# Kernel optimization log

Measured on AMD Instinct MI355X. Metric: run time of the kernel, lower is better.

The kernel has to match this reference:

```python
import jax, jax.numpy as jnp
import numpy as np
from jax.scipy.special import erfinv

EMBED = 384
HEADS = 6
HEAD_DIM = EMBED // HEADS  # 64
N_FREQS = HEAD_DIM // 2    # 32
SEQ = 1025                 # 1 CLS + 32*32 patches
POS_DIM = 2
MIN_FREQ, MAX_FREQ = 0.1, 1000.0


def _phi(m: int) -> float:
    x = 2.0
    for _ in range(10):
        x = (1.0 + x) ** (1.0 / (m + 1.0))
    return x


def _uniform_directions(n: int, d: int) -> jnp.ndarray:
    # golden-ratio quasi-random directions, normalized (matches uniform_directions_jax)
    g = _phi(d)
    alpha = (1.0 / g) ** jnp.arange(1, d + 1, dtype=jnp.float32)
    i = jnp.arange(1, n + 1, dtype=jnp.float32)[:, None]
    z = jnp.fmod(i * alpha, 1.0)
    dirs = erfinv(2.0 * z - 1.0)
    return dirs / jnp.linalg.norm(dirs, axis=1, keepdims=True)


def _rope_freqs() -> jnp.ndarray:  # [h, F, P]
    omega = MIN_FREQ * (MAX_FREQ / MIN_FREQ) ** jnp.linspace(0.0, 1.0, N_FREQS)
    dirs = _uniform_directions(HEADS * N_FREQS, POS_DIM).reshape(HEADS, N_FREQS, POS_DIM)
    return dirs * omega.reshape(1, N_FREQS, 1)


def _coords_2d() -> jnp.ndarray:  # [S, 2], CLS at origin, patches in [-1,1]^2
    n = int(np.sqrt(SEQ - 1))  # 32
    yy, xx = jnp.meshgrid(jnp.arange(n), jnp.arange(n), indexing='ij')
    xf = xx.flatten().astype(jnp.float32) / (n - 1) * 2 - 1
    yf = yy.flatten().astype(jnp.float32) / (n - 1) * 2 - 1
    patch = jnp.stack([xf, yf], axis=1)
    return jnp.concatenate([jnp.zeros((1, 2), jnp.float32), patch], axis=0)


def _apply_rope(t_bshd, freqs_hFP, coords_SP):
    # theta: [S, h, F]
    theta = jnp.einsum('hfp,sp->shf', freqs_hFP, coords_SP)
    cos, sin = jnp.cos(theta), jnp.sin(theta)  # broadcast over batch
    x1, y1 = jnp.split(t_bshd, 2, axis=-1)     # [b,s,h,F] each
    return jnp.concatenate([x1 * cos - y1 * sin, x1 * sin + y1 * cos], axis=-1)


def setup_inputs() -> dict:
    key = jax.random.key(0)
    ks = jax.random.split(key, 6)
    scale = 1.0 / np.sqrt(EMBED)
    return {
        'x':  jax.random.normal(ks[0], (16, SEQ, EMBED), jnp.float32),
        'Wq': jax.random.normal(ks[1], (EMBED, EMBED), jnp.float32) * scale,
        'Wk': jax.random.normal(ks[2], (EMBED, EMBED), jnp.float32) * scale,
        'Wv': jax.random.normal(ks[3], (EMBED, EMBED), jnp.float32) * scale,
        'Wo': jax.random.normal(ks[4], (EMBED, EMBED), jnp.float32) * scale,
        'bo': jnp.zeros((EMBED,), jnp.float32),
    }


def reference(x, Wq, Wk, Wv, Wo, bo):
    b, s, e = x.shape
    freqs = _rope_freqs()   # constant buffers
    coords = _coords_2d()
    q = (x @ Wq).reshape(b, s, HEADS, HEAD_DIM)
    k = (x @ Wk).reshape(b, s, HEADS, HEAD_DIM)
    v = (x @ Wv).reshape(b, s, HEADS, HEAD_DIM)
    q = _apply_rope(q, freqs, coords)
    k = _apply_rope(k, freqs, coords)
    scores = jnp.einsum('blhd,bmhd->bhlm', q, k) / np.sqrt(HEAD_DIM)
    attn = jax.nn.softmax(scores, axis=-1)
    out = jnp.einsum('bhlm,bmhd->blhd', attn, v).reshape(b, s, e)
    return out @ Wo + bo
```

## Files before the change

### kernel.cpp

```cpp
#include <hip/hip_runtime.h>
#include <hip/hip_bf16.h>
#include <math.h>

#define EMBED 384
#define HEADS 6
#define HD    64
#define NF    32
#define SEQ   1025
#define SEQP  1088
#define BATCH 16
#define MTOT  (BATCH*SEQ)
#define NCHUNK 17
#define LSTRIDE 72
#define GSTR 40

typedef __bf16 bf16x8 __attribute__((ext_vector_type(8)));
typedef __bf16 bf16x4 __attribute__((ext_vector_type(4)));
typedef float  f32x4  __attribute__((ext_vector_type(4)));

#define MFMA_BF16(A,B,C) __builtin_amdgcn_mfma_f32_16x16x32_bf16((A),(B),(C),0,0,0)

__device__ __forceinline__ __bf16 f2bf(float f){
    __hip_bfloat16 h = __float2bfloat16(f);
    return *reinterpret_cast<__bf16*>(&h);
}

__global__ __launch_bounds__(256) void x_to_bf16_kernel(
    const float* __restrict__ x, __hip_bfloat16* __restrict__ xb)
{
    const int n4 = MTOT*EMBED/4;
    int i = blockIdx.x*256 + threadIdx.x;
    if (i < n4){
        float4 v = *reinterpret_cast<const float4*>(x + (size_t)i*4);
        bf16x4 b; b[0]=f2bf(v.x); b[1]=f2bf(v.y); b[2]=f2bf(v.z); b[3]=f2bf(v.w);
        *reinterpret_cast<bf16x4*>(reinterpret_cast<__bf16*>(xb) + (size_t)i*4) = b;
    }
}

__global__ __launch_bounds__(256) void transpose_w_kernel(
    const float* __restrict__ Wq, const float* __restrict__ Wk,
    const float* __restrict__ Wv, const float* __restrict__ Wo,
    __hip_bfloat16* __restrict__ Wt)
{
    __shared__ float tile[64][65];
    const int mat = blockIdx.z;
    const float* W = (mat==0)?Wq:(mat==1)?Wk:(mat==2)?Wv:Wo;
    const int k0 = blockIdx.x*64, n0 = blockIdx.y*64;
    const int c = threadIdx.x & 63, rq = threadIdx.x >> 6;
    #pragma unroll
    for (int i = 0; i < 16; ++i){
        int row = rq*16 + i;
        tile[row][c] = W[(size_t)(k0+row)*EMBED + n0 + c];
    }
    __syncthreads();
    #pragma unroll
    for (int i = 0; i < 16; ++i){
        int nr = rq*16 + i;
        Wt[((size_t)mat*EMBED + n0 + nr)*EMBED + k0 + c] = __float2bfloat16(tile[c][nr]);
    }
}

__device__ __forceinline__ float erfinv_f(float x){
    float w = -log1pf(-x*x);
    float p;
    if (w < 5.0f){
        w -= 2.5f;
        p = 2.81022636e-08f;
        p = fmaf(p, w, 3.43273939e-07f);
        p = fmaf(p, w, -3.5233877e-06f);
        p = fmaf(p, w, -4.39150654e-06f);
        p = fmaf(p, w, 0.00021858087f);
        p = fmaf(p, w, -0.00125372503f);
        p = fmaf(p, w, -0.00417768164f);
        p = fmaf(p, w, 0.246640727f);
        p = fmaf(p, w, 1.50140941f);
    } else {
        w = sqrtf(w) - 3.0f;
        p = -0.000200214257f;
        p = fmaf(p, w, 0.000100950558f);
        p = fmaf(p, w, 0.00134934322f);
        p = fmaf(p, w, -0.00367342844f);
        p = fmaf(p, w, 0.00573950773f);
        p = fmaf(p, w, -0.0076224613f);
        p = fmaf(p, w, 0.00943887047f);
        p = fmaf(p, w, 1.00167406f);
        p = fmaf(p, w, 2.83297682f);
    }
    return p * x;
}

__global__ void rope_tables_kernel(float* __restrict__ cos_t, float* __restrict__ sin_t){
    int idx = blockIdx.x * blockDim.x + threadIdx.x;
    if (idx >= SEQ*HEADS*NF) return;
    int f  = idx & (NF-1);
    int hf = idx / NF;
    int h  = hf % HEADS;
    int s  = hf / HEADS;

    double xd = 2.0;
    #pragma unroll
    for (int it = 0; it < 10; ++it) xd = cbrt(1.0 + xd);
    float a1 = (float)(1.0 / xd);
    float a2 = a1 * a1;

    float fi = (float)(h*NF + f + 1);
    float z1 = fmodf(fi * a1, 1.0f);
    float z2 = fmodf(fi * a2, 1.0f);
    float d1 = erfinv_f(2.0f*z1 - 1.0f);
    float d2 = erfinv_f(2.0f*z2 - 1.0f);
    float inv = 1.0f / sqrtf(d1*d1 + d2*d2);
    d1 *= inv; d2 *= inv;

    float omega = 0.1f * powf(10000.0f, (float)f / 31.0f);
    float fx = d1 * omega, fy = d2 * omega;

    float cx = 0.0f, cy = 0.0f;
    if (s > 0){
        int pi = s - 1;
        cx = (float)(pi & 31) / 31.0f * 2.0f - 1.0f;
        cy = (float)(pi >> 5) / 31.0f * 2.0f - 1.0f;
    }
    float theta = fx*cx + fy*cy;
    float sv, cv;
    sincosf(theta, &sv, &cv);
    cos_t[idx] = cv;
    sin_t[idx] = sv;
}

__global__ __launch_bounds__(256, 3) void qkv_rope_kernel(
    const __hip_bfloat16* __restrict__ xb_,
    const __hip_bfloat16* __restrict__ Wt,
    const float* __restrict__ cos_t,
    const float* __restrict__ sin_t,
    __hip_bfloat16* __restrict__ qbuf,
    __hip_bfloat16* __restrict__ kbuf,
    __hip_bfloat16* __restrict__ vbuf)
{
    __shared__ __align__(16) __bf16 xs[128*GSTR];
    __shared__ __align__(16) __bf16 bt[128*GSTR];
    const int tid = threadIdx.x;
    const int m0 = blockIdx.x * 128;
    const int j  = blockIdx.y;
    const __bf16* xb = reinterpret_cast<const __bf16*>(xb_);
    const __bf16* wt = reinterpret_cast<const __bf16*>(Wt);

    int soff[2], arow[2], brow[2];
    #pragma unroll
    for (int i = 0; i < 2; ++i){
        int g = tid + i*256;
        int row = g >> 2, kc = g & 3;
        soff[i] = row*GSTR + kc*8;
        int am = m0 + row; if (am > MTOT-1) am = MTOT-1;
        arow[i] = am;
        brow[i] = j*128 + row;
    }

    bf16x8 ar[2], br[2];
    #pragma unroll
    for (int i = 0; i < 2; ++i){
        int g = tid + i*256, kc = g & 3;
        ar[i] = *reinterpret_cast<const bf16x8*>(xb + (size_t)arow[i]*EMBED + kc*8);
        br[i] = *reinterpret_cast<const bf16x8*>(wt + (size_t)brow[i]*EMBED + kc*8);
    }

    const int w = tid >> 6;
    const int lane = tid & 63;
    const int quad = lane >> 4, low = lane & 15;
    const int mh = w >> 1, nh = w & 1;
    const int mw0 = m0 + mh*64;

    f32x4 acc[4][4] = {};
    for (int kb = 0; kb < 12; ++kb){
        __syncthreads();
        #pragma unroll
        for (int i = 0; i < 2; ++i){
            *reinterpret_cast<bf16x8*>(&xs[soff[i]]) = ar[i];
            *reinterpret_cast<bf16x8*>(&bt[soff[i]]) = br[i];
        }
        __syncthreads();
        if (kb < 11){
            const int k1 = (kb+1)*32;
            #pragma unroll
            for (int i = 0; i < 2; ++i){
                int g = tid + i*256, kc = g & 3;
                ar[i] = *reinterpret_cast<const bf16x8*>(xb + (size_t)arow[i]*EMBED + k1 + kc*8);
                br[i] = *reinterpret_cast<const bf16x8*>(wt + (size_t)brow[i]*EMBED + k1 + kc*8);
            }
        }
        bf16x8 af[4], bfr[4];
        #pragma unroll
        for (int mt = 0; mt < 4; ++mt)
            af[mt] = *reinterpret_cast<const bf16x8*>(&xs[(mh*64 + mt*16 + low)*GSTR + quad*8]);
        #pragma unroll
        for (int t = 0; t < 4; ++t)
            bfr[t] = *reinterpret_cast<const bf16x8*>(&bt[(nh*64 + t*16 + low)*GSTR + quad*8]);
        #pragma unroll
        for (int t = 0; t < 4; ++t)
            #pragma unroll
            for (int mt = 0; mt < 4; ++mt)
                acc[mt][t] = MFMA_BF16(af[mt], bfr[t], acc[mt][t]);
    }

    const int n64 = j*2 + nh;
    const int mat = n64 / 6;
    const int h   = n64 % 6;

    if (mat == 2){
        #pragma unroll
        for (int mt = 0; mt < 4; ++mt)
            #pragma unroll
            for (int t = 0; t < 4; ++t)
                #pragma unroll
                for (int r = 0; r < 4; ++r){
                    int m = mw0 + mt*16 + quad*4 + r;
                    if (m < MTOT){
                        int b = m / SEQ, s = m % SEQ;
                        vbuf[((size_t)(b*HEADS + h)*SEQ + s)*HD + t*16 + low] = __float2bfloat16(acc[mt][t][r]);
                    }
                }
    } else {
        __hip_bfloat16* ob = (mat == 0) ? qbuf : kbuf;
        const float qs_ = (mat == 0) ? 0.125f : 1.0f;
        #pragma unroll
        for (int mt = 0; mt < 4; ++mt)
            #pragma unroll
            for (int t = 0; t < 2; ++t)
                #pragma unroll
                for (int r = 0; r < 4; ++r){
                    int m = mw0 + mt*16 + quad*4 + r;
                    if (m < MTOT){
                        int b = m / SEQ, s = m % SEQ;
                        int f = t*16 + low;
                        float cv = cos_t[(s*HEADS + h)*NF + f];
                        float sv = sin_t[(s*HEADS + h)*NF + f];
                        float x1 = acc[mt][t][r];
                        float y1 = acc[mt][t+2][r];
                        size_t base = ((size_t)(b*HEADS + h)*SEQ + s)*HD;
                        ob[base + f]      = __float2bfloat16((x1*cv - y1*sv)*qs_);
                        ob[base + NF + f] = __float2bfloat16((x1*sv + y1*cv)*qs_);
                    }
                }
    }
}

__global__ __launch_bounds__(256) void vt_transpose_kernel(
    const __hip_bfloat16* __restrict__ v, __hip_bfloat16* __restrict__ vt)
{
    __shared__ __bf16 tileT[64*72];
    const int tid = threadIdx.x;
    const int bh = blockIdx.x;
    const int s0 = blockIdx.y * 64;
    const __bf16* vb = reinterpret_cast<const __bf16*>(v) + (size_t)bh*SEQ*HD;
    #pragma unroll
    for (int i = 0; i < 2; ++i){
        int ch = tid + i*256;
        int srow = ch >> 3, dg = ch & 7;
        int s = s0 + srow; if (s > SEQ-1) s = SEQ-1;
        bf16x8 val = *reinterpret_cast<const bf16x8*>(vb + (size_t)s*HD + dg*8);
        #pragma unroll
        for (int e = 0; e < 8; ++e)
            tileT[(dg*8 + e)*72 + srow] = val[e];
    }
    __syncthreads();
    __bf16* ot = reinterpret_cast<__bf16*>(vt) + (size_t)bh*HD*SEQP;
    #pragma unroll
    for (int i = 0; i < 2; ++i){
        int ch = tid + i*256;
        int d = ch >> 3, sg = ch & 7;
        bf16x8 val = *reinterpret_cast<const bf16x8*>(&tileT[d*72 + sg*8]);
        *reinterpret_cast<bf16x8*>(ot + (size_t)d*SEQP + s0 + sg*8) = val;
    }
}

__global__ __launch_bounds__(256, 4) void attn_kernel(
    const __hip_bfloat16* __restrict__ qbuf,
    const __hip_bfloat16* __restrict__ kbuf,
    const __hip_bfloat16* __restrict__ vtbuf,
    __hip_bfloat16* __restrict__ aout)
{
    __shared__ __align__(16) __bf16 kls[64*LSTRIDE];
    __shared__ __align__(16) __bf16 vls[64*LSTRIDE];
    __shared__ __align__(16) __bf16 pls[4][32*LSTRIDE];
    const int tid  = threadIdx.x;
    const int w    = tid >> 6;
    const int lane = tid & 63;
    const int quad = lane >> 4, low = lane & 15;
    const int id = blockIdx.x;
    const int bh = id % 96;
    const int qt = id / 96;
    const int b = bh / HEADS, h = bh % HEADS;
    const __bf16* qb = reinterpret_cast<const __bf16*>(qbuf);
    const __bf16* kb = reinterpret_cast<const __bf16*>(kbuf);
    const __bf16* vt = reinterpret_cast<const __bf16*>(vtbuf);
    const size_t base   = (size_t)bh * SEQ * HD;
    const size_t vtbase = (size_t)bh * HD * SEQP;
    const int q0 = qt*128 + w*32;

    int srow[2], sgk[2], soff[2];
    #pragma unroll
    for (int i = 0; i < 2; ++i){
        int ch = tid + i*256;
        srow[i] = ch >> 3; sgk[i] = ch & 7;
        soff[i] = srow[i]*LSTRIDE + sgk[i]*8;
    }

    bf16x8 bq[2][2];
    #pragma unroll
    for (int nt = 0; nt < 2; ++nt){
        int qs = q0 + nt*16 + low; if (qs > SEQ-1) qs = SEQ-1;
        #pragma unroll
        for (int ks = 0; ks < 2; ++ks)
            bq[nt][ks] = *reinterpret_cast<const bf16x8*>(qb + base + (size_t)qs*HD + ks*32 + quad*8);
    }

    bf16x8 kr[2], vr[2];
    #pragma unroll
    for (int i = 0; i < 2; ++i){
        int kk = srow[i]; if (kk > SEQ-1) kk = SEQ-1;
        kr[i] = *reinterpret_cast<const bf16x8*>(kb + base + (size_t)kk*HD + sgk[i]*8);
        vr[i] = *reinterpret_cast<const bf16x8*>(vt + vtbase + (size_t)srow[i]*SEQP + sgk[i]*8);
    }

    f32x4 o[4][2] = {};
    float l_i[2] = {0.f, 0.f};

    for (int c = 0; c < NCHUNK; ++c){
        const int c0 = c*64;
        __syncthreads();
        #pragma unroll
        for (int i = 0; i < 2; ++i){
            *reinterpret_cast<bf16x8*>(&kls[soff[i]]) = kr[i];
            *reinterpret_cast<bf16x8*>(&vls[soff[i]]) = vr[i];
        }
        __syncthreads();
        if (c + 1 < NCHUNK){
            const int c1 = c0 + 64;
            #pragma unroll
            for (int i = 0; i < 2; ++i){
                int kk = c1 + srow[i]; if (kk > SEQ-1) kk = SEQ-1;
                kr[i] = *reinterpret_cast<const bf16x8*>(kb + base + (size_t)kk*HD + sgk[i]*8);
                vr[i] = *reinterpret_cast<const bf16x8*>(vt + vtbase + (size_t)srow[i]*SEQP + c1 + sgk[i]*8);
            }
        }
        f32x4 st[4][2] = {};
        #pragma unroll
        for (int kt = 0; kt < 4; ++kt)
            #pragma unroll
            for (int ks = 0; ks < 2; ++ks){
                bf16x8 ak = *reinterpret_cast<const bf16x8*>(&kls[(kt*16 + low)*LSTRIDE + ks*32 + quad*8]);
                #pragma unroll
                for (int nt = 0; nt < 2; ++nt)
                    st[kt][nt] = MFMA_BF16(ak, bq[nt][ks], st[kt][nt]);
            }
        if (c0 + 64 > SEQ){
            #pragma unroll
            for (int kt = 0; kt < 4; ++kt)
                #pragma unroll
                for (int r = 0; r < 4; ++r){
                    int key = c0 + kt*16 + quad*4 + r;
                    if (key >= SEQ){ st[kt][0][r] = -1e30f; st[kt][1][r] = -1e30f; }
                }
        }
        #pragma unroll
        for (int nt = 0; nt < 2; ++nt)
            #pragma unroll
            for (int kt = 0; kt < 4; ++kt)
                #pragma unroll
                for (int r = 0; r < 4; ++r){
                    float p = __expf(st[kt][nt][r]);
                    st[kt][nt][r] = p;
                    l_i[nt] += p;
                }
        #pragma unroll
        for (int nt = 0; nt < 2; ++nt)
            #pragma unroll
            for (int kt = 0; kt < 4; ++kt){
                bf16x4 pk;
                pk[0] = f2bf(st[kt][nt][0]); pk[1] = f2bf(st[kt][nt][1]);
                pk[2] = f2bf(st[kt][nt][2]); pk[3] = f2bf(st[kt][nt][3]);
                *reinterpret_cast<bf16x4*>(&pls[w][(nt*16 + low)*LSTRIDE + kt*16 + quad*4]) = pk;
            }
        asm volatile("s_waitcnt lgkmcnt(0)" ::: "memory");
        #pragma unroll
        for (int ks2 = 0; ks2 < 2; ++ks2){
            bf16x8 bp[2];
            #pragma unroll
            for (int nt = 0; nt < 2; ++nt)
                bp[nt] = *reinterpret_cast<const bf16x8*>(&pls[w][(nt*16 + low)*LSTRIDE + ks2*32 + quad*8]);
            #pragma unroll
            for (int dt = 0; dt < 4; ++dt){
                bf16x8 av = *reinterpret_cast<const bf16x8*>(&vls[(dt*16 + low)*LSTRIDE + ks2*32 + quad*8]);
                #pragma unroll
                for (int nt = 0; nt < 2; ++nt)
                    o[dt][nt] = MFMA_BF16(av, bp[nt], o[dt][nt]);
            }
        }
    }

    #pragma unroll
    for (int nt = 0; nt < 2; ++nt){
        l_i[nt] += __shfl_xor(l_i[nt], 16, 64);
        l_i[nt] += __shfl_xor(l_i[nt], 32, 64);
    }
    #pragma unroll
    for (int nt = 0; nt < 2; ++nt){
        int s = q0 + nt*16 + low;
        if (s < SEQ){
            float inv = 1.0f / l_i[nt];
            #pragma unroll
            for (int dt = 0; dt < 4; ++dt){
                bf16x4 ov;
                #pragma unroll
                for (int r = 0; r < 4; ++r) ov[r] = f2bf(o[dt][nt][r]*inv);
                *reinterpret_cast<bf16x4*>(
                    reinterpret_cast<__bf16*>(aout) + ((size_t)b*SEQ + s)*EMBED + h*HD + dt*16 + quad*4) = ov;
            }
        }
    }
}

__global__ __launch_bounds__(256, 3) void outproj_kernel(
    const __hip_bfloat16* __restrict__ a,
    const __hip_bfloat16* __restrict__ Wt,
    const float* __restrict__ bo,
    float* __restrict__ out)
{
    __shared__ __align__(16) __bf16 xs[128*GSTR];
    __shared__ __align__(16) __bf16 bt[128*GSTR];
    const int tid = threadIdx.x;
    const int m0 = blockIdx.x * 128;
    const int j  = blockIdx.y;
    const __bf16* ab = reinterpret_cast<const __bf16*>(a);
    const __bf16* wt = reinterpret_cast<const __bf16*>(Wt) + (size_t)3*EMBED*EMBED;

    int soff[2], arow[2], brow[2];
    #pragma unroll
    for (int i = 0; i < 2; ++i){
        int g = tid + i*256;
        int row = g >> 2, kc = g & 3;
        soff[i] = row*GSTR + kc*8;
        int am = m0 + row; if (am > MTOT-1) am = MTOT-1;
        arow[i] = am;
        brow[i] = j*128 + row;
    }
    bf16x8 ar[2], br[2];
    #pragma unroll
    for (int i = 0; i < 2; ++i){
        int g = tid + i*256, kc = g & 3;
        ar[i] = *reinterpret_cast<const bf16x8*>(ab + (size_t)arow[i]*EMBED + kc*8);
        br[i] = *reinterpret_cast<const bf16x8*>(wt + (size_t)brow[i]*EMBED + kc*8);
    }

    const int w = tid >> 6;
    const int lane = tid & 63;
    const int quad = lane >> 4, low = lane & 15;
    const int mh = w >> 1, nh = w & 1;
    const int mw0 = m0 + mh*64;
    const int n0 = j*128 + nh*64;

    f32x4 acc[4][4] = {};
    for (int kb = 0; kb < 12; ++kb){
        __syncthreads();
        #pragma unroll
        for (int i = 0; i < 2; ++i){
            *reinterpret_cast<bf16x8*>(&xs[soff[i]]) = ar[i];
            *reinterpret_cast<bf16x8*>(&bt[soff[i]]) = br[i];
        }
        __syncthreads();
        if (kb < 11){
            const int k1 = (kb+1)*32;
            #pragma unroll
            for (int i = 0; i < 2; ++i){
                int g = tid + i*256, kc = g & 3;
                ar[i] = *reinterpret_cast<const bf16x8*>(ab + (size_t)arow[i]*EMBED + k1 + kc*8);
                br[i] = *reinterpret_cast<const bf16x8*>(wt + (size_t)brow[i]*EMBED + k1 + kc*8);
            }
        }
        bf16x8 af[4], bfr[4];
        #pragma unroll
        for (int mt = 0; mt < 4; ++mt)
            af[mt] = *reinterpret_cast<const bf16x8*>(&xs[(mh*64 + mt*16 + low)*GSTR + quad*8]);
        #pragma unroll
        for (int t = 0; t < 4; ++t)
            bfr[t] = *reinterpret_cast<const bf16x8*>(&bt[(nh*64 + t*16 + low)*GSTR + quad*8]);
        #pragma unroll
        for (int t = 0; t < 4; ++t)
            #pragma unroll
            for (int mt = 0; mt < 4; ++mt)
                acc[mt][t] = MFMA_BF16(af[mt], bfr[t], acc[mt][t]);
    }

    #pragma unroll
    for (int t = 0; t < 4; ++t){
        const int n = n0 + t*16 + low;
        const float bias = bo[n];
        #pragma unroll
        for (int mt = 0; mt < 4; ++mt)
            #pragma unroll
            for (int r = 0; r < 4; ++r){
                const int m = mw0 + mt*16 + quad*4 + r;
                if (m < MTOT) out[(size_t)m*EMBED + n] = acc[mt][t][r] + bias;
            }
    }
}

extern "C" void kernel_launch(void* const* d_in, const int* in_sizes, int n_in,
                              void* d_out, int out_size, void* d_ws, size_t ws_size,
                              hipStream_t stream)
{
    const float* x  = (const float*)d_in[0];
    const float* Wq = (const float*)d_in[1];
    const float* Wk = (const float*)d_in[2];
    const float* Wv = (const float*)d_in[3];
    const float* Wo = (const float*)d_in[4];
    const float* bo = (const float*)d_in[5];
    float* out = (float*)d_out;

    const size_t NE = (size_t)MTOT * EMBED;
    const size_t VT = (size_t)BATCH*HEADS*HD*SEQP;
    char* ws = (char*)d_ws;
    size_t off = 0;
    __hip_bfloat16* qbuf = (__hip_bfloat16*)(ws + off); off += 2*NE;
    __hip_bfloat16* kbuf = (__hip_bfloat16*)(ws + off); off += 2*NE;
    __hip_bfloat16* abuf = (__hip_bfloat16*)(ws + off); off += 2*NE;
    __hip_bfloat16* vbuf = (__hip_bfloat16*)(ws + off); off += 2*NE;
    __hip_bfloat16* xbuf = (__hip_bfloat16*)(ws + off); off += 2*NE;
    __hip_bfloat16* vt   = (__hip_bfloat16*)(ws + off); off += 2*VT;
    __hip_bfloat16* Wt   = (__hip_bfloat16*)(ws + off); off += (size_t)4*EMBED*EMBED*2;
    float* cos_t = (float*)(ws + off); off += (size_t)SEQ*HEADS*NF*4;
    float* sin_t = (float*)(ws + off); off += (size_t)SEQ*HEADS*NF*4;

    x_to_bf16_kernel<<<dim3((MTOT*EMBED/4 + 255)/256), dim3(256), 0, stream>>>(x, xbuf);
    transpose_w_kernel<<<dim3(6,6,4), dim3(256), 0, stream>>>(Wq, Wk, Wv, Wo, Wt);
    rope_tables_kernel<<<dim3((SEQ*HEADS*NF + 255)/256), dim3(256), 0, stream>>>(cos_t, sin_t);
    qkv_rope_kernel<<<dim3((MTOT + 127)/128, 9), dim3(256), 0, stream>>>(xbuf, Wt, cos_t, sin_t, qbuf, kbuf, vbuf);
    vt_transpose_kernel<<<dim3(96, 17), dim3(256), 0, stream>>>(vbuf, vt);
    attn_kernel<<<dim3(864), dim3(256), 0, stream>>>(qbuf, kbuf, vt, abuf);
    outproj_kernel<<<dim3((MTOT + 127)/128, 3), dim3(256), 0, stream>>>(abuf, Wt, bo, out);
}
```

Baseline: 210.3 us.

## Load K/V fragments directly from global memory and use exp2 softmax

The attention kernel no longer stages K and V tiles through shared memory with block-wide barriers. Each wave now loads its MFMA operand fragments for K and V^T straight from global memory into registers. The softmax switches from __expf to exp2f, with log2(e) folded into the Q scaling in the projection kernel, and the row-sum is reduced with vector adds. This removes LDS traffic and both __syncthreads per chunk. In exchange, every wave issues redundant global loads for the same K/V chunk, there is no longer a prefetch of the next chunk, and the K row index is no longer clamped, so the last chunk can read past the end of the buffer.

```diff
diff --git a/kernel.cpp b/kernel.cpp
--- a/kernel.cpp
+++ b/kernel.cpp
@@ -220,7 +220,7 @@
                 }
     } else {
         __hip_bfloat16* ob = (mat == 0) ? qbuf : kbuf;
-        const float qs_ = (mat == 0) ? 0.125f : 1.0f;
+        const float qs_ = (mat == 0) ? 0.125f*1.44269504089f : 1.0f;
         #pragma unroll
         for (int mt = 0; mt < 4; ++mt)
             #pragma unroll
@@ -278,8 +278,6 @@
     const __hip_bfloat16* __restrict__ vtbuf,
     __hip_bfloat16* __restrict__ aout)
 {
-    __shared__ __align__(16) __bf16 kls[64*LSTRIDE];
-    __shared__ __align__(16) __bf16 vls[64*LSTRIDE];
     __shared__ __align__(16) __bf16 pls[4][32*LSTRIDE];
     const int tid  = threadIdx.x;
     const int w    = tid >> 6;
@@ -296,14 +294,6 @@
     const size_t vtbase = (size_t)bh * HD * SEQP;
     const int q0 = qt*128 + w*32;
 
-    int srow[2], sgk[2], soff[2];
-    #pragma unroll
-    for (int i = 0; i < 2; ++i){
-        int ch = tid + i*256;
-        srow[i] = ch >> 3; sgk[i] = ch & 7;
-        soff[i] = srow[i]*LSTRIDE + sgk[i]*8;
-    }
-
     bf16x8 bq[2][2];
     #pragma unroll
     for (int nt = 0; nt < 2; ++nt){
@@ -313,45 +303,33 @@
             bq[nt][ks] = *reinterpret_cast<const bf16x8*>(qb + base + (size_t)qs*HD + ks*32 + quad*8);
     }
 
-    bf16x8 kr[2], vr[2];
-    #pragma unroll
-    for (int i = 0; i < 2; ++i){
-        int kk = srow[i]; if (kk > SEQ-1) kk = SEQ-1;
-        kr[i] = *reinterpret_cast<const bf16x8*>(kb + base + (size_t)kk*HD + sgk[i]*8);
-        vr[i] = *reinterpret_cast<const bf16x8*>(vt + vtbase + (size_t)srow[i]*SEQP + sgk[i]*8);
-    }
-
     f32x4 o[4][2] = {};
     float l_i[2] = {0.f, 0.f};
 
     for (int c = 0; c < NCHUNK; ++c){
         const int c0 = c*64;
-        __syncthreads();
-        #pragma unroll
-        for (int i = 0; i < 2; ++i){
-            *reinterpret_cast<bf16x8*>(&kls[soff[i]]) = kr[i];
-            *reinterpret_cast<bf16x8*>(&vls[soff[i]]) = vr[i];
-        }
-        __syncthreads();
-        if (c + 1 < NCHUNK){
-            const int c1 = c0 + 64;
-            #pragma unroll
-            for (int i = 0; i < 2; ++i){
-                int kk = c1 + srow[i]; if (kk > SEQ-1) kk = SEQ-1;
-                kr[i] = *reinterpret_cast<const bf16x8*>(kb + base + (size_t)kk*HD + sgk[i]*8);
-                vr[i] = *reinterpret_cast<const bf16x8*>(vt + vtbase + (size_t)srow[i]*SEQP + c1 + sgk[i]*8);
-            }
-        }
+        bf16x8 kf[4][2];
+        #pragma unroll
+        for (int kt = 0; kt < 4; ++kt)
+            #pragma unroll
+            for (int ks = 0; ks < 2; ++ks)
+                kf[kt][ks] = *reinterpret_cast<const bf16x8*>(
+                    kb + base + (size_t)(c0 + kt*16 + low)*HD + ks*32 + quad*8);
         f32x4 st[4][2] = {};
         #pragma unroll
         for (int kt = 0; kt < 4; ++kt)
             #pragma unroll
-            for (int ks = 0; ks < 2; ++ks){
-                bf16x8 ak = *reinterpret_cast<const bf16x8*>(&kls[(kt*16 + low)*LSTRIDE + ks*32 + quad*8]);
+            for (int ks = 0; ks < 2; ++ks)
                 #pragma unroll
                 for (int nt = 0; nt < 2; ++nt)
-                    st[kt][nt] = MFMA_BF16(ak, bq[nt][ks], st[kt][nt]);
-            }
+                    st[kt][nt] = MFMA_BF16(kf[kt][ks], bq[nt][ks], st[kt][nt]);
+        bf16x8 vf[4][2];
+        #pragma unroll
+        for (int dt = 0; dt < 4; ++dt)
+            #pragma unroll
+            for (int ks2 = 0; ks2 < 2; ++ks2)
+                vf[dt][ks2] = *reinterpret_cast<const bf16x8*>(
+                    vt + vtbase + (size_t)(dt*16 + low)*SEQP + c0 + ks2*32 + quad*8);
         if (c0 + 64 > SEQ){
             #pragma unroll
             for (int kt = 0; kt < 4; ++kt)
@@ -362,15 +340,17 @@
                 }
         }
         #pragma unroll
-        for (int nt = 0; nt < 2; ++nt)
+        for (int nt = 0; nt < 2; ++nt){
             #pragma unroll
             for (int kt = 0; kt < 4; ++kt)
                 #pragma unroll
-                for (int r = 0; r < 4; ++r){
-                    float p = __expf(st[kt][nt][r]);
-                    st[kt][nt][r] = p;
-                    l_i[nt] += p;
-                }
+                for (int r = 0; r < 4; ++r)
+                    st[kt][nt][r] = exp2f(st[kt][nt][r]);
+            f32x4 ps = st[0][nt] + st[1][nt];
+            f32x4 ps2 = st[2][nt] + st[3][nt];
+            ps = ps + ps2;
+            l_i[nt] += (ps[0] + ps[1]) + (ps[2] + ps[3]);
+        }
         #pragma unroll
         for (int nt = 0; nt < 2; ++nt)
             #pragma unroll
@@ -388,12 +368,10 @@
             for (int nt = 0; nt < 2; ++nt)
                 bp[nt] = *reinterpret_cast<const bf16x8*>(&pls[w][(nt*16 + low)*LSTRIDE + ks2*32 + quad*8]);
             #pragma unroll
-            for (int dt = 0; dt < 4; ++dt){
-                bf16x8 av = *reinterpret_cast<const bf16x8*>(&vls[(dt*16 + low)*LSTRIDE + ks2*32 + quad*8]);
+            for (int dt = 0; dt < 4; ++dt)
                 #pragma unroll
                 for (int nt = 0; nt < 2; ++nt)
-                    o[dt][nt] = MFMA_BF16(av, bp[nt], o[dt][nt]);
-            }
+                    o[dt][nt] = MFMA_BF16(vf[dt][ks2], bp[nt], o[dt][nt]);
         }
     }
 
```

New measurement: 306.6 us. 45.8% more time.

## Rewrite QKV GEMM to load fragments directly from global, vectorize epilogue, use exp2

Applied to the files above, without the earlier changes.

The QKV projection kernel drops its LDS staging and block-level syncs. Each wave now loads its MFMA fragments straight from global memory, with operands swapped so each lane holds four consecutive outputs, which allows vectorized bf16x4 stores and float4 cos/sin loads in the RoPE epilogue. The grid is re-tiled to 18 head-blocks by 256 rows. Q is pre-scaled by log2(e) so attention can use exp2f with a tree-reduced row sum. The trade-off is more redundant global and L2 traffic, since fragments are no longer shared across waves.

```diff
diff --git a/kernel.cpp b/kernel.cpp
--- a/kernel.cpp
+++ b/kernel.cpp
@@ -127,7 +127,7 @@
     sin_t[idx] = sv;
 }
 
-__global__ __launch_bounds__(256, 3) void qkv_rope_kernel(
+__global__ __launch_bounds__(256) void qkv_rope_kernel(
     const __hip_bfloat16* __restrict__ xb_,
     const __hip_bfloat16* __restrict__ Wt,
     const float* __restrict__ cos_t,
@@ -136,110 +136,88 @@
     __hip_bfloat16* __restrict__ kbuf,
     __hip_bfloat16* __restrict__ vbuf)
 {
-    __shared__ __align__(16) __bf16 xs[128*GSTR];
-    __shared__ __align__(16) __bf16 bt[128*GSTR];
     const int tid = threadIdx.x;
-    const int m0 = blockIdx.x * 128;
-    const int j  = blockIdx.y;
-    const __bf16* xb = reinterpret_cast<const __bf16*>(xb_);
-    const __bf16* wt = reinterpret_cast<const __bf16*>(Wt);
-
-    int soff[2], arow[2], brow[2];
-    #pragma unroll
-    for (int i = 0; i < 2; ++i){
-        int g = tid + i*256;
-        int row = g >> 2, kc = g & 3;
-        soff[i] = row*GSTR + kc*8;
-        int am = m0 + row; if (am > MTOT-1) am = MTOT-1;
-        arow[i] = am;
-        brow[i] = j*128 + row;
-    }
-
-    bf16x8 ar[2], br[2];
-    #pragma unroll
-    for (int i = 0; i < 2; ++i){
-        int g = tid + i*256, kc = g & 3;
-        ar[i] = *reinterpret_cast<const bf16x8*>(xb + (size_t)arow[i]*EMBED + kc*8);
-        br[i] = *reinterpret_cast<const bf16x8*>(wt + (size_t)brow[i]*EMBED + kc*8);
-    }
-
     const int w = tid >> 6;
     const int lane = tid & 63;
     const int quad = lane >> 4, low = lane & 15;
-    const int mh = w >> 1, nh = w & 1;
-    const int mw0 = m0 + mh*64;
+    const int n64 = blockIdx.x;
+    const int mat = n64 / 6, h = n64 % 6;
+    const int m0 = blockIdx.y*256 + w*64;
+    const __bf16* xb = reinterpret_cast<const __bf16*>(xb_);
+    const __bf16* wt = reinterpret_cast<const __bf16*>(Wt);
+    const int nbase = n64*64;
+
+    int mrow[4];
+    #pragma unroll
+    for (int mt = 0; mt < 4; ++mt){
+        int m = m0 + mt*16 + low;
+        mrow[mt] = (m > MTOT-1) ? MTOT-1 : m;
+    }
 
     f32x4 acc[4][4] = {};
+    #pragma unroll
     for (int kb = 0; kb < 12; ++kb){
-        __syncthreads();
-        #pragma unroll
-        for (int i = 0; i < 2; ++i){
-            *reinterpret_cast<bf16x8*>(&xs[soff[i]]) = ar[i];
-            *reinterpret_cast<bf16x8*>(&bt[soff[i]]) = br[i];
-        }
-        __syncthreads();
-        if (kb < 11){
-            const int k1 = (kb+1)*32;
-            #pragma unroll
-            for (int i = 0; i < 2; ++i){
-                int g = tid + i*256, kc = g & 3;
-                ar[i] = *reinterpret_cast<const bf16x8*>(xb + (size_t)arow[i]*EMBED + k1 + kc*8);
-                br[i] = *reinterpret_cast<const bf16x8*>(wt + (size_t)brow[i]*EMBED + k1 + kc*8);
-            }
-        }
-        bf16x8 af[4], bfr[4];
+        const int k0 = kb*32;
+        bf16x8 af[4], bf_[4];
+        #pragma unroll
+        for (int t = 0; t < 4; ++t)
+            af[t] = *reinterpret_cast<const bf16x8*>(
+                wt + (size_t)(nbase + t*16 + low)*EMBED + k0 + quad*8);
         #pragma unroll
         for (int mt = 0; mt < 4; ++mt)
-            af[mt] = *reinterpret_cast<const bf16x8*>(&xs[(mh*64 + mt*16 + low)*GSTR + quad*8]);
+            bf_[mt] = *reinterpret_cast<const bf16x8*>(
+                xb + (size_t)mrow[mt]*EMBED + k0 + quad*8);
         #pragma unroll
         for (int t = 0; t < 4; ++t)
-            bfr[t] = *reinterpret_cast<const bf16x8*>(&bt[(nh*64 + t*16 + low)*GSTR + quad*8]);
-        #pragma unroll
-        for (int t = 0; t < 4; ++t)
             #pragma unroll
             for (int mt = 0; mt < 4; ++mt)
-                acc[mt][t] = MFMA_BF16(af[mt], bfr[t], acc[mt][t]);
-    }
-
-    const int n64 = j*2 + nh;
-    const int mat = n64 / 6;
-    const int h   = n64 % 6;
+                acc[t][mt] = MFMA_BF16(af[t], bf_[mt], acc[t][mt]);
+    }
 
     if (mat == 2){
         #pragma unroll
-        for (int mt = 0; mt < 4; ++mt)
-            #pragma unroll
-            for (int t = 0; t < 4; ++t)
-                #pragma unroll
-                for (int r = 0; r < 4; ++r){
-                    int m = mw0 + mt*16 + quad*4 + r;
-                    if (m < MTOT){
-                        int b = m / SEQ, s = m % SEQ;
-                        vbuf[((size_t)(b*HEADS + h)*SEQ + s)*HD + t*16 + low] = __float2bfloat16(acc[mt][t][r]);
-                    }
+        for (int mt = 0; mt < 4; ++mt){
+            int m = m0 + mt*16 + low;
+            if (m < MTOT){
+                int b = m / SEQ, s = m % SEQ;
+                __bf16* vb = reinterpret_cast<__bf16*>(vbuf) + ((size_t)(b*HEADS + h)*SEQ + s)*HD;
+                #pragma unroll
+                for (int t = 0; t < 4; ++t){
+                    bf16x4 pk;
+                    #pragma unroll
+                    for (int r = 0; r < 4; ++r) pk[r] = f2bf(acc[t][mt][r]);
+                    *reinterpret_cast<bf16x4*>(vb + t*16 + quad*4) = pk;
                 }
+            }
+        }
     } else {
         __hip_bfloat16* ob = (mat == 0) ? qbuf : kbuf;
-        const float qs_ = (mat == 0) ? 0.125f : 1.0f;
-        #pragma unroll
-        for (int mt = 0; mt < 4; ++mt)
-            #pragma unroll
-            for (int t = 0; t < 2; ++t)
-                #pragma unroll
-                for (int r = 0; r < 4; ++r){
-                    int m = mw0 + mt*16 + quad*4 + r;
-                    if (m < MTOT){
-                        int b = m / SEQ, s = m % SEQ;
-                        int f = t*16 + low;
-                        float cv = cos_t[(s*HEADS + h)*NF + f];
-                        float sv = sin_t[(s*HEADS + h)*NF + f];
-                        float x1 = acc[mt][t][r];
-                        float y1 = acc[mt][t+2][r];
-                        size_t base = ((size_t)(b*HEADS + h)*SEQ + s)*HD;
-                        ob[base + f]      = __float2bfloat16((x1*cv - y1*sv)*qs_);
-                        ob[base + NF + f] = __float2bfloat16((x1*sv + y1*cv)*qs_);
+        const float qs_ = (mat == 0) ? 0.125f*1.44269504089f : 1.0f;
+        #pragma unroll
+        for (int mt = 0; mt < 4; ++mt){
+            int m = m0 + mt*16 + low;
+            if (m < MTOT){
+                int b = m / SEQ, s = m % SEQ;
+                __bf16* op = reinterpret_cast<__bf16*>(ob) + ((size_t)(b*HEADS + h)*SEQ + s)*HD;
+                const int tb = (s*HEADS + h)*NF;
+                #pragma unroll
+                for (int t = 0; t < 2; ++t){
+                    const int f0 = t*16 + quad*4;
+                    f32x4 cv = *reinterpret_cast<const f32x4*>(cos_t + tb + f0);
+                    f32x4 sv = *reinterpret_cast<const f32x4*>(sin_t + tb + f0);
+                    bf16x4 o1, o2;
+                    #pragma unroll
+                    for (int r = 0; r < 4; ++r){
+                        float x1 = acc[t][mt][r];
+                        float y1 = acc[t+2][mt][r];
+                        o1[r] = f2bf((x1*cv[r] - y1*sv[r])*qs_);
+                        o2[r] = f2bf((x1*sv[r] + y1*cv[r])*qs_);
                     }
+                    *reinterpret_cast<bf16x4*>(op + f0)      = o1;
+                    *reinterpret_cast<bf16x4*>(op + NF + f0) = o2;
                 }
+            }
+        }
     }
 }
 
@@ -362,15 +340,15 @@
                 }
         }
         #pragma unroll
-        for (int nt = 0; nt < 2; ++nt)
+        for (int nt = 0; nt < 2; ++nt){
             #pragma unroll
             for (int kt = 0; kt < 4; ++kt)
                 #pragma unroll
-                for (int r = 0; r < 4; ++r){
-                    float p = __expf(st[kt][nt][r]);
-                    st[kt][nt][r] = p;
-                    l_i[nt] += p;
-                }
+                for (int r = 0; r < 4; ++r)
+                    st[kt][nt][r] = exp2f(st[kt][nt][r]);
+            f32x4 ps = (st[0][nt] + st[1][nt]) + (st[2][nt] + st[3][nt]);
+            l_i[nt] += (ps[0] + ps[1]) + (ps[2] + ps[3]);
+        }
         #pragma unroll
         for (int nt = 0; nt < 2; ++nt)
             #pragma unroll
@@ -533,7 +511,7 @@
     x_to_bf16_kernel<<<dim3((MTOT*EMBED/4 + 255)/256), dim3(256), 0, stream>>>(x, xbuf);
     transpose_w_kernel<<<dim3(6,6,4), dim3(256), 0, stream>>>(Wq, Wk, Wv, Wo, Wt);
     rope_tables_kernel<<<dim3((SEQ*HEADS*NF + 255)/256), dim3(256), 0, stream>>>(cos_t, sin_t);
-    qkv_rope_kernel<<<dim3((MTOT + 127)/128, 9), dim3(256), 0, stream>>>(xbuf, Wt, cos_t, sin_t, qbuf, kbuf, vbuf);
+    qkv_rope_kernel<<<dim3(18, (MTOT + 255)/256), dim3(256), 0, stream>>>(xbuf, Wt, cos_t, sin_t, qbuf, kbuf, vbuf);
     vt_transpose_kernel<<<dim3(96, 17), dim3(256), 0, stream>>>(vbuf, vt);
     attn_kernel<<<dim3(864), dim3(256), 0, stream>>>(qbuf, kbuf, vt, abuf);
     outproj_kernel<<<dim3((MTOT + 127)/128, 3), dim3(256), 0, stream>>>(abuf, Wt, bo, out);
```

Result: slower. 254.5 us (+21.0%).
